# Optimization experiments

Measured on AMD Instinct MI355X. Metric: run time of the kernel, lower is better.

## Reference

```python
import jax, jax.numpy as jnp
import numpy as np
from jax import lax

EPS = 1e-20


def _conv(x, w, pad):
    # x: [B,C,H,W], w: [O,I,kh,kw]
    return lax.conv_general_dilated(
        x, w, window_strides=(1, 1), padding=[(pad, pad), (pad, pad)],
        dimension_numbers=('NCHW', 'OIHW', 'NCHW'))


def _softplus10(p):
    # F.softplus(p, beta=10) = log(1 + exp(10 p)) / 10
    return jax.nn.softplus(10.0 * p) / 10.0


def _nconv(data, conf, w_p, b, pad):
    """Normalized convolution: conv(data*conf)/conv(conf) + bias; cout = conv(conf)/sum(W)."""
    w = _softplus10(w_p)                       # enforce positivity
    denom = _conv(conf, w, pad)                # [B,O,H,W]
    nomin = _conv(data * conf, w, pad)
    out = nomin / (denom + EPS) + b[None, :, None, None]
    s = jnp.sum(w, axis=(1, 2, 3))             # per-out-channel kernel sum
    cout = denom / s[None, :, None, None]
    return out, cout


def _pool_ds2(conf, x):
    """2x2 max-pool on conf (returning conf/4) and gather of x at the argmax positions
    (vectorized equivalent of the torch double for-loop unpool-gather)."""
    B, C, H, W = conf.shape
    cw = conf.reshape(B, C, H // 2, 2, W // 2, 2).transpose(0, 1, 2, 4, 3, 5).reshape(B, C, H // 2, W // 2, 4)
    xw = x.reshape(B, C, H // 2, 2, W // 2, 2).transpose(0, 1, 2, 4, 3, 5).reshape(B, C, H // 2, W // 2, 4)
    idx = jnp.argmax(cw, axis=-1)              # first-max, row-major window order (matches torch)
    c_ds = jnp.take_along_axis(cw, idx[..., None], axis=-1)[..., 0] / 4.0
    x_ds = jnp.take_along_axis(xw, idx[..., None], axis=-1)[..., 0]
    return c_ds, x_ds


def _up2(x):
    return jnp.repeat(jnp.repeat(x, 2, axis=2), 2, axis=3)


def _forward(x0, c0, params):
    (w1, b1, w2, b2, w3, b3, w4, b4, w5, b5, w6, b6, w7, b7) = params
    x1, c1 = _nconv(x0, c0, w1, b1, 2)
    x1, c1 = _nconv(x1, c1, w2, b2, 2)
    x1, c1 = _nconv(x1, c1, w3, b3, 2)

    c1_ds, x1_ds = _pool_ds2(c1, x1)
    x2_ds, c2_ds = _nconv(x1_ds, c1_ds, w2, b2, 2)
    x2_ds, c2_ds = _nconv(x2_ds, c2_ds, w3, b3, 2)

    c2_dss, x2_dss = _pool_ds2(c2_ds, x2_ds)
    x3_ds, c3_ds = _nconv(x2_dss, c2_dss, w2, b2, 2)

    c3_dss, x3_dss = _pool_ds2(c3_ds, x3_ds)
    x4_ds, c4_ds = _nconv(x3_dss, c3_dss, w2, b2, 2)

    x4, c4 = _up2(x4_ds), _up2(c4_ds)
    x34_ds, c34_ds = _nconv(jnp.concatenate((x3_ds, x4), 1), jnp.concatenate((c3_ds, c4), 1), w4, b4, 1)

    x34, c34 = _up2(x34_ds), _up2(c34_ds)
    x23_ds, c23_ds = _nconv(jnp.concatenate((x2_ds, x34), 1), jnp.concatenate((c2_ds, c34), 1), w5, b5, 1)

    x23, c23 = _up2(x23_ds), _up2(c23_ds)
    xout, cout = _nconv(jnp.concatenate((x23, x1), 1), jnp.concatenate((c23, c1), 1), w6, b6, 1)
    xout, cout = _nconv(xout, cout, w7, b7, 0)
    return xout, cout


def setup_inputs() -> dict:
    key = jax.random.key(0)
    ks = jax.random.split(key, 16)
    B, C, H, W = 16, 1, 352, 1216
    nc = 2  # in_ch * num_channels
    x0 = jax.random.uniform(ks[0], (B, C, H, W), jnp.float32)
    c0 = jax.random.uniform(ks[1], (B, C, H, W), jnp.float32)

    def wp(k, shape):
        # weight_p = softplus(kaiming-uniform init); sample a positive-ish param directly
        return jax.random.uniform(k, shape, jnp.float32, 0.02, 0.3)

    inp = {
        'x0': x0, 'c0': c0,
        'w1': wp(ks[2], (nc, C, 5, 5)),       'b1': jnp.full((nc,), 0.01, jnp.float32),
        'w2': wp(ks[3], (nc, nc, 5, 5)),      'b2': jnp.full((nc,), 0.01, jnp.float32),
        'w3': wp(ks[4], (nc, nc, 5, 5)),      'b3': jnp.full((nc,), 0.01, jnp.float32),
        'w4': wp(ks[5], (nc, 2 * nc, 3, 3)),  'b4': jnp.full((nc,), 0.01, jnp.float32),
        'w5': wp(ks[6], (nc, 2 * nc, 3, 3)),  'b5': jnp.full((nc,), 0.01, jnp.float32),
        'w6': wp(ks[7], (nc, 2 * nc, 3, 3)),  'b6': jnp.full((nc,), 0.01, jnp.float32),
        'w7': wp(ks[8], (1, nc, 1, 1)),       'b7': jnp.full((1,), 0.01, jnp.float32),
    }
    return inp


def reference(x0, c0, w1, b1, w2, b2, w3, b3, w4, b4, w5, b5, w6, b6, w7, b7):
    return _forward(x0, c0, (w1, b1, w2, b2, w3, b3, w4, b4, w5, b5, w6, b6, w7, b7))
```

## Files before the change

kernel.cpp:

```cpp
#include <hip/hip_runtime.h>
#include <hip/hip_bf16.h>

#define EPSF 1e-20f
typedef __hip_bfloat16 bf16;
typedef unsigned int u32;

__device__ __forceinline__ float rcpf_(float v) { return __builtin_amdgcn_rcpf(v); }
__device__ __forceinline__ float bits2f(u32 b) { union { u32 i; float f; } u; u.i = b; return u.f; }
__device__ __forceinline__ float lo2f(u32 v) { return bits2f(v << 16); }
__device__ __forceinline__ float hi2f(u32 v) { return bits2f(v & 0xffff0000u); }
__device__ __forceinline__ u32 f2us(float f) {
    bf16 h = __float2bfloat16(f);
    unsigned short s;
    __builtin_memcpy(&s, &h, 2);
    return (u32)s;
}
__device__ __forceinline__ uint2 packpx(float x0, float c0, float x1, float c1) {
    return make_uint2(f2us(x0) | (f2us(c0) << 16), f2us(x1) | (f2us(c1) << 16));
}
__device__ __forceinline__ float4 unpk(uint2 v) {
    float x0 = lo2f(v.x), c0 = hi2f(v.x), x1 = lo2f(v.y), c1 = hi2f(v.y);
    return make_float4(x0 * c0, c0, x1 * c1, c1);
}

#define B_ 16
#define H1 352
#define W1 1216
#define H2 176
#define W2 608
#define H3 88
#define W3 304
#define H4 44
#define W4 152

__global__ void prep_weights(const float* w1, const float* w2, const float* w3,
                             const float* w4, const float* w5, const float* w6,
                             const float* w7, float* wb) {
    const float* ptrs[7] = {w1, w2, w3, w4, w5, w6, w7};
    const int ns[7]   = {50, 100, 100, 72, 72, 72, 2};
    const int offs[7] = {0, 96, 256, 416, 544, 672, 800};
    for (int it = 0; it < 7; ++it)
        for (int i = threadIdx.x; i < ns[it]; i += blockDim.x) {
            float z = 10.f * ptrs[it][i];
            float sp = (z > 20.f) ? z : log1pf(expf(z));
            wb[offs[it] + i] = sp * 0.1f;
        }
    __syncthreads();
    if (threadIdx.x == 0) {
        const int souts[7] = {2, 2, 2, 2, 2, 2, 1};
        const int klen[7]  = {25, 50, 50, 36, 36, 36, 2};
        const int soff[7]  = {64, 224, 384, 512, 640, 768, 804};
        for (int it = 0; it < 7; ++it)
            for (int o = 0; o < souts[it]; ++o) {
                float s = 0.f;
                for (int i = 0; i < klen[it]; ++i) s += wb[offs[it] + o * klen[it] + i];
                wb[soff[it] + o] = s;
            }
        for (int o = 0; o < 2; ++o) {
            wb[808 + o] = 1.f / wb[64 + o];
            wb[810 + o] = 1.f / wb[224 + o];
            wb[812 + o] = 1.f / wb[384 + o];
            wb[814 + o] = 1.f / wb[512 + o];
            wb[816 + o] = 1.f / wb[640 + o];
            wb[818 + o] = 1.f / wb[768 + o];
        }
        wb[820] = 1.f / wb[804];
    }
}

#define TDIM 32

__global__ __launch_bounds__(256) void fused_l1pool(
    const float* __restrict__ x0g, const float* __restrict__ c0g,
    const float* __restrict__ wb,
    const float* __restrict__ b1, const float* __restrict__ b2, const float* __restrict__ b3,
    uint2* __restrict__ Apk, uint2* __restrict__ P1pk) {

    __shared__ float4 A1[40 * 41];
    __shared__ float4 U4[36 * 37];
    float2* U2 = (float2*)U4;

    const int tid = threadIdx.x;
    const int base_h = blockIdx.y * TDIM;
    const int base_w = blockIdx.x * TDIM;
    const int b = blockIdx.z;
    const float* xp = x0g + (long)b * (H1 * W1);
    const float* cp = c0g + (long)b * (H1 * W1);

    for (int i = tid; i < 44 * 44; i += 256) {
        int r = i / 44, c = i % 44;
        int gh = base_h - 6 + r, gw = base_w - 6 + c;
        float xv = 0.f, cv = 0.f;
        if (gh >= 0 && gh < H1 && gw >= 0 && gw < W1) {
            long o = (long)gh * W1 + gw;
            xv = xp[o]; cv = cp[o];
        }
        U2[r * 45 + c] = make_float2(xv * cv, cv);
    }
    __syncthreads();

    {
        const float is0 = wb[808], is1 = wb[809];
        const float bb0 = b1[0], bb1 = b1[1];
        for (int i = tid; i < 400; i += 256) {
            int qr = i / 20, qc = i % 20;
            int r0 = 2 * qr, c0 = 2 * qc;
            float acc[2][2][4];
            #pragma unroll
            for (int a = 0; a < 2; ++a)
                #pragma unroll
                for (int o = 0; o < 2; ++o)
                    #pragma unroll
                    for (int k = 0; k < 4; ++k) acc[a][o][k] = 0.f;
            #pragma unroll
            for (int tr = 0; tr < 6; ++tr) {
                float2 t[6];
                #pragma unroll
                for (int j = 0; j < 6; ++j) t[j] = U2[(r0 + tr) * 45 + c0 + j];
                #pragma unroll
                for (int orr = 0; orr < 2; ++orr) {
                    const int dh = tr - orr;
                    if (dh < 0 || dh > 4) continue;
                    #pragma unroll
                    for (int dw = 0; dw < 5; ++dw) {
                        float wA = wb[dh * 5 + dw];
                        float wB = wb[25 + dh * 5 + dw];
                        #pragma unroll
                        for (int oc = 0; oc < 2; ++oc) {
                            float2 v = t[dw + oc];
                            acc[orr][oc][0] = fmaf(wA, v.x, acc[orr][oc][0]);
                            acc[orr][oc][1] = fmaf(wA, v.y, acc[orr][oc][1]);
                            acc[orr][oc][2] = fmaf(wB, v.x, acc[orr][oc][2]);
                            acc[orr][oc][3] = fmaf(wB, v.y, acc[orr][oc][3]);
                        }
                    }
                }
            }
            #pragma unroll
            for (int orr = 0; orr < 2; ++orr)
                #pragma unroll
                for (int oc = 0; oc < 2; ++oc) {
                    int r = r0 + orr, cc = c0 + oc;
                    int gh = base_h - 4 + r, gw = base_w - 4 + cc;
                    float4 out = make_float4(0.f, 0.f, 0.f, 0.f);
                    if (gh >= 0 && gh < H1 && gw >= 0 && gw < W1) {
                        float n0 = acc[orr][oc][0], d0 = acc[orr][oc][1];
                        float n1 = acc[orr][oc][2], d1 = acc[orr][oc][3];
                        float c0v = d0 * is0, x0v = n0 * rcpf_(d0 + EPSF) + bb0;
                        float c1v = d1 * is1, x1v = n1 * rcpf_(d1 + EPSF) + bb1;
                        out = make_float4(x0v * c0v, c0v, x1v * c1v, c1v);
                    }
                    A1[r * 41 + cc] = out;
                }
        }
    }
    __syncthreads();

    {
        const float is0 = wb[810], is1 = wb[811];
        const float bb0 = b2[0], bb1 = b2[1];
        for (int i = tid; i < 324; i += 256) {
            int qr = i / 18, qc = i % 18;
            int r0 = 2 * qr, c0 = 2 * qc;
            float acc[2][2][4];
            #pragma unroll
            for (int a = 0; a < 2; ++a)
                #pragma unroll
                for (int o = 0; o < 2; ++o)
                    #pragma unroll
                    for (int k = 0; k < 4; ++k) acc[a][o][k] = 0.f;
            #pragma unroll
            for (int tr = 0; tr < 6; ++tr) {
                float4 t[6];
                #pragma unroll
                for (int j = 0; j < 6; ++j) t[j] = A1[(r0 + tr) * 41 + c0 + j];
                #pragma unroll
                for (int orr = 0; orr < 2; ++orr) {
                    const int dh = tr - orr;
                    if (dh < 0 || dh > 4) continue;
                    #pragma unroll
                    for (int dw = 0; dw < 5; ++dw) {
                        const int k = dh * 5 + dw;
                        float wa0 = wb[96 + k],  wc0 = wb[121 + k];
                        float wa1 = wb[146 + k], wc1 = wb[171 + k];
                        #pragma unroll
                        for (int oc = 0; oc < 2; ++oc) {
                            float4 v = t[dw + oc];
                            acc[orr][oc][0] = fmaf(wa0, v.x, fmaf(wc0, v.z, acc[orr][oc][0]));
                            acc[orr][oc][1] = fmaf(wa0, v.y, fmaf(wc0, v.w, acc[orr][oc][1]));
                            acc[orr][oc][2] = fmaf(wa1, v.x, fmaf(wc1, v.z, acc[orr][oc][2]));
                            acc[orr][oc][3] = fmaf(wa1, v.y, fmaf(wc1, v.w, acc[orr][oc][3]));
                        }
                    }
                }
            }
            #pragma unroll
            for (int orr = 0; orr < 2; ++orr)
                #pragma unroll
                for (int oc = 0; oc < 2; ++oc) {
                    int r = r0 + orr, cc = c0 + oc;
                    int gh = base_h - 2 + r, gw = base_w - 2 + cc;
                    float4 out = make_float4(0.f, 0.f, 0.f, 0.f);
                    if (gh >= 0 && gh < H1 && gw >= 0 && gw < W1) {
                        float n0 = acc[orr][oc][0], d0 = acc[orr][oc][1];
                        float n1 = acc[orr][oc][2], d1 = acc[orr][oc][3];
                        float c0v = d0 * is0, x0v = n0 * rcpf_(d0 + EPSF) + bb0;
                        float c1v = d1 * is1, x1v = n1 * rcpf_(d1 + EPSF) + bb1;
                        out = make_float4(x0v * c0v, c0v, x1v * c1v, c1v);
                    }
                    U4[r * 37 + cc] = out;
                }
        }
    }
    __syncthreads();

    {
        const float is0 = wb[812], is1 = wb[813];
        const float bb0 = b3[0], bb1 = b3[1];
        const int pr = tid >> 4, pc = tid & 15;
        const int r0 = 2 * pr, c0 = 2 * pc;
        float acc[2][2][4];
        #pragma unroll
        for (int a = 0; a < 2; ++a)
            #pragma unroll
            for (int o = 0; o < 2; ++o)
                #pragma unroll
                for (int k = 0; k < 4; ++k) acc[a][o][k] = 0.f;
        #pragma unroll
        for (int tr = 0; tr < 6; ++tr) {
            float4 t[6];
            #pragma unroll
            for (int j = 0; j < 6; ++j) t[j] = U4[(r0 + tr) * 37 + c0 + j];
            #pragma unroll
            for (int orr = 0; orr < 2; ++orr) {
                const int dh = tr - orr;
                if (dh < 0 || dh > 4) continue;
                #pragma unroll
                for (int dw = 0; dw < 5; ++dw) {
                    const int k = dh * 5 + dw;
                    float wa0 = wb[256 + k], wc0 = wb[281 + k];
                    float wa1 = wb[306 + k], wc1 = wb[331 + k];
                    #pragma unroll
                    for (int oc = 0; oc < 2; ++oc) {
                        float4 v = t[dw + oc];
                        acc[orr][oc][0] = fmaf(wa0, v.x, fmaf(wc0, v.z, acc[orr][oc][0]));
                        acc[orr][oc][1] = fmaf(wa0, v.y, fmaf(wc0, v.w, acc[orr][oc][1]));
                        acc[orr][oc][2] = fmaf(wa1, v.x, fmaf(wc1, v.z, acc[orr][oc][2]));
                        acc[orr][oc][3] = fmaf(wa1, v.y, fmaf(wc1, v.w, acc[orr][oc][3]));
                    }
                }
            }
        }
        float xv[2][4], cv[2][4];
        #pragma unroll
        for (int orr = 0; orr < 2; ++orr)
            #pragma unroll
            for (int oc = 0; oc < 2; ++oc) {
                int q = orr * 2 + oc;
                float n0 = acc[orr][oc][0], d0 = acc[orr][oc][1];
                float n1 = acc[orr][oc][2], d1 = acc[orr][oc][3];
                xv[0][q] = n0 * rcpf_(d0 + EPSF) + bb0;
                xv[1][q] = n1 * rcpf_(d1 + EPSF) + bb1;
                cv[0][q] = d0 * is0;
                cv[1][q] = d1 * is1;
            }
        int fh = base_h + r0, fw = base_w + c0;
        int ph = (base_h >> 1) + pr, pw = (base_w >> 1) + pc;
        uint2 q00 = packpx(xv[0][0], cv[0][0], xv[1][0], cv[1][0]);
        uint2 q01 = packpx(xv[0][1], cv[0][1], xv[1][1], cv[1][1]);
        uint2 q10 = packpx(xv[0][2], cv[0][2], xv[1][2], cv[1][2]);
        uint2 q11 = packpx(xv[0][3], cv[0][3], xv[1][3], cv[1][3]);
        long o0 = (long)b * (H1 * W1) + (long)fh * W1 + fw;
        *reinterpret_cast<uint4*>(Apk + o0)      = make_uint4(q00.x, q00.y, q01.x, q01.y);
        *reinterpret_cast<uint4*>(Apk + o0 + W1) = make_uint4(q10.x, q10.y, q11.x, q11.y);
        float cm0 = cv[0][0], xs0 = xv[0][0];
        if (cv[0][1] > cm0) { cm0 = cv[0][1]; xs0 = xv[0][1]; }
        if (cv[0][2] > cm0) { cm0 = cv[0][2]; xs0 = xv[0][2]; }
        if (cv[0][3] > cm0) { cm0 = cv[0][3]; xs0 = xv[0][3]; }
        float cm1 = cv[1][0], xs1 = xv[1][0];
        if (cv[1][1] > cm1) { cm1 = cv[1][1]; xs1 = xv[1][1]; }
        if (cv[1][2] > cm1) { cm1 = cv[1][2]; xs1 = xv[1][2]; }
        if (cv[1][3] > cm1) { cm1 = cv[1][3]; xs1 = xv[1][3]; }
        P1pk[(long)b * (H2 * W2) + (long)ph * W2 + pw] =
            packpx(xs0, cm0 * 0.25f, xs1, cm1 * 0.25f);
    }
}

__global__ __launch_bounds__(256) void fused_l2(
    const uint2* __restrict__ P1pk, const float* __restrict__ wb,
    const float* __restrict__ b2, const float* __restrict__ b3,
    uint2* __restrict__ Dpk, uint2* __restrict__ P2pk) {

    __shared__ float4 T0[40 * 41];
    __shared__ float4 T1[36 * 37];

    const int tid = threadIdx.x;
    const int base_h = blockIdx.y * 32;
    const int base_w = blockIdx.x * 32;
    const int b = blockIdx.z;
    const long pl = (long)H2 * W2;
    const uint2* ip = P1pk + (long)b * pl;

    for (int i = tid; i < 40 * 40; i += 256) {
        int r = i / 40, c = i % 40;
        int gh = base_h - 4 + r, gw = base_w - 4 + c;
        float4 v = make_float4(0.f, 0.f, 0.f, 0.f);
        if (gh >= 0 && gh < H2 && gw >= 0 && gw < W2)
            v = unpk(ip[(long)gh * W2 + gw]);
        T0[r * 41 + c] = v;
    }
    __syncthreads();

    {
        const float is0 = wb[810], is1 = wb[811];
        const float bb0 = b2[0], bb1 = b2[1];
        for (int i = tid; i < 324; i += 256) {
            int qr = i / 18, qc = i % 18;
            int r0 = 2 * qr, c0 = 2 * qc;
            float acc[2][2][4];
            #pragma unroll
            for (int a = 0; a < 2; ++a)
                #pragma unroll
                for (int o = 0; o < 2; ++o)
                    #pragma unroll
                    for (int k = 0; k < 4; ++k) acc[a][o][k] = 0.f;
            #pragma unroll
            for (int tr = 0; tr < 6; ++tr) {
                float4 t[6];
                #pragma unroll
                for (int j = 0; j < 6; ++j) t[j] = T0[(r0 + tr) * 41 + c0 + j];
                #pragma unroll
                for (int orr = 0; orr < 2; ++orr) {
                    const int dh = tr - orr;
                    if (dh < 0 || dh > 4) continue;
                    #pragma unroll
                    for (int dw = 0; dw < 5; ++dw) {
                        const int k = dh * 5 + dw;
                        float wa0 = wb[96 + k],  wc0 = wb[121 + k];
                        float wa1 = wb[146 + k], wc1 = wb[171 + k];
                        #pragma unroll
                        for (int oc = 0; oc < 2; ++oc) {
                            float4 v = t[dw + oc];
                            acc[orr][oc][0] = fmaf(wa0, v.x, fmaf(wc0, v.z, acc[orr][oc][0]));
                            acc[orr][oc][1] = fmaf(wa0, v.y, fmaf(wc0, v.w, acc[orr][oc][1]));
                            acc[orr][oc][2] = fmaf(wa1, v.x, fmaf(wc1, v.z, acc[orr][oc][2]));
                            acc[orr][oc][3] = fmaf(wa1, v.y, fmaf(wc1, v.w, acc[orr][oc][3]));
                        }
                    }
                }
            }
            #pragma unroll
            for (int orr = 0; orr < 2; ++orr)
                #pragma unroll
                for (int oc = 0; oc < 2; ++oc) {
                    int r = r0 + orr, cc = c0 + oc;
                    int gh = base_h - 2 + r, gw = base_w - 2 + cc;
                    float4 out = make_float4(0.f, 0.f, 0.f, 0.f);
                    if (gh >= 0 && gh < H2 && gw >= 0 && gw < W2) {
                        float n0 = acc[orr][oc][0], d0 = acc[orr][oc][1];
                        float n1 = acc[orr][oc][2], d1 = acc[orr][oc][3];
                        float c0v = d0 * is0, x0v = n0 * rcpf_(d0 + EPSF) + bb0;
                        float c1v = d1 * is1, x1v = n1 * rcpf_(d1 + EPSF) + bb1;
                        out = make_float4(x0v * c0v, c0v, x1v * c1v, c1v);
                    }
                    T1[r * 37 + cc] = out;
                }
        }
    }
    __syncthreads();

    {
        const float is0 = wb[812], is1 = wb[813];
        const float bb0 = b3[0], bb1 = b3[1];
        const int pr = tid >> 4, pc = tid & 15;
        const int r0 = 2 * pr, c0 = 2 * pc;
        float acc[2][2][4];
        #pragma unroll
        for (int a = 0; a < 2; ++a)
            #pragma unroll
            for (int o = 0; o < 2; ++o)
                #pragma unroll
                for (int k = 0; k < 4; ++k) acc[a][o][k] = 0.f;
        #pragma unroll
        for (int tr = 0; tr < 6; ++tr) {
            float4 t[6];
            #pragma unroll
            for (int j = 0; j < 6; ++j) t[j] = T1[(r0 + tr) * 37 + c0 + j];
            #pragma unroll
            for (int orr = 0; orr < 2; ++orr) {
                const int dh = tr - orr;
                if (dh < 0 || dh > 4) continue;
                #pragma unroll
                for (int dw = 0; dw < 5; ++dw) {
                    const int k = dh * 5 + dw;
                    float wa0 = wb[256 + k], wc0 = wb[281 + k];
                    float wa1 = wb[306 + k], wc1 = wb[331 + k];
                    #pragma unroll
                    for (int oc = 0; oc < 2; ++oc) {
                        float4 v = t[dw + oc];
                        acc[orr][oc][0] = fmaf(wa0, v.x, fmaf(wc0, v.z, acc[orr][oc][0]));
                        acc[orr][oc][1] = fmaf(wa0, v.y, fmaf(wc0, v.w, acc[orr][oc][1]));
                        acc[orr][oc][2] = fmaf(wa1, v.x, fmaf(wc1, v.z, acc[orr][oc][2]));
                        acc[orr][oc][3] = fmaf(wa1, v.y, fmaf(wc1, v.w, acc[orr][oc][3]));
                    }
                }
            }
        }
        int fh = base_h + r0, fw = base_w + c0;
        if (fh < H2) {
            float xv[2][4], cv[2][4];
            #pragma unroll
            for (int orr = 0; orr < 2; ++orr)
                #pragma unroll
                for (int oc = 0; oc < 2; ++oc) {
                    int q = orr * 2 + oc;
                    float n0 = acc[orr][oc][0], d0 = acc[orr][oc][1];
                    float n1 = acc[orr][oc][2], d1 = acc[orr][oc][3];
                    xv[0][q] = n0 * rcpf_(d0 + EPSF) + bb0;
                    xv[1][q] = n1 * rcpf_(d1 + EPSF) + bb1;
                    cv[0][q] = d0 * is0;
                    cv[1][q] = d1 * is1;
                }
            uint2 q00 = packpx(xv[0][0], cv[0][0], xv[1][0], cv[1][0]);
            uint2 q01 = packpx(xv[0][1], cv[0][1], xv[1][1], cv[1][1]);
            uint2 q10 = packpx(xv[0][2], cv[0][2], xv[1][2], cv[1][2]);
            uint2 q11 = packpx(xv[0][3], cv[0][3], xv[1][3], cv[1][3]);
            long o0 = (long)b * pl + (long)fh * W2 + fw;
            *reinterpret_cast<uint4*>(Dpk + o0)      = make_uint4(q00.x, q00.y, q01.x, q01.y);
            *reinterpret_cast<uint4*>(Dpk + o0 + W2) = make_uint4(q10.x, q10.y, q11.x, q11.y);
            float cm0 = cv[0][0], xs0 = xv[0][0];
            if (cv[0][1] > cm0) { cm0 = cv[0][1]; xs0 = xv[0][1]; }
            if (cv[0][2] > cm0) { cm0 = cv[0][2]; xs0 = xv[0][2]; }
            if (cv[0][3] > cm0) { cm0 = cv[0][3]; xs0 = xv[0][3]; }
            float cm1 = cv[1][0], xs1 = xv[1][0];
            if (cv[1][1] > cm1) { cm1 = cv[1][1]; xs1 = xv[1][1]; }
            if (cv[1][2] > cm1) { cm1 = cv[1][2]; xs1 = xv[1][2]; }
            if (cv[1][3] > cm1) { cm1 = cv[1][3]; xs1 = xv[1][3]; }
            int ph = (base_h >> 1) + pr, pw = (base_w >> 1) + pc;
            P2pk[(long)b * (H3 * W3) + (long)ph * W3 + pw] =
                packpx(xs0, cm0 * 0.25f, xs1, cm1 * 0.25f);
        }
    }
}

__global__ __launch_bounds__(256) void fused_l3(
    const uint2* __restrict__ P2pk, const float* __restrict__ wb,
    const float* __restrict__ b2,
    uint2* __restrict__ Gpk, uint2* __restrict__ P3pk) {

    __shared__ float4 T0[36 * 37];

    const int tid = threadIdx.x;
    const int base_h = blockIdx.y * 32;
    const int base_w = blockIdx.x * 32;
    const int b = blockIdx.z;
    const long pl = (long)H3 * W3;
    const uint2* ip = P2pk + (long)b * pl;

    for (int i = tid; i < 36 * 36; i += 256) {
        int r = i / 36, c = i % 36;
        int gh = base_h - 2 + r, gw = base_w - 2 + c;
        float4 v = make_float4(0.f, 0.f, 0.f, 0.f);
        if (gh >= 0 && gh < H3 && gw >= 0 && gw < W3)
            v = unpk(ip[(long)gh * W3 + gw]);
        T0[r * 37 + c] = v;
    }
    __syncthreads();

    {
        const float is0 = wb[810], is1 = wb[811];
        const float bb0 = b2[0], bb1 = b2[1];
        const int pr = tid >> 4, pc = tid & 15;
        const int r0 = 2 * pr, c0 = 2 * pc;
        float acc[2][2][4];
        #pragma unroll
        for (int a = 0; a < 2; ++a)
            #pragma unroll
            for (int o = 0; o < 2; ++o)
                #pragma unroll
                for (int k = 0; k < 4; ++k) acc[a][o][k] = 0.f;
        #pragma unroll
        for (int tr = 0; tr < 6; ++tr) {
            float4 t[6];
            #pragma unroll
            for (int j = 0; j < 6; ++j) t[j] = T0[(r0 + tr) * 37 + c0 + j];
            #pragma unroll
            for (int orr = 0; orr < 2; ++orr) {
                const int dh = tr - orr;
                if (dh < 0 || dh > 4) continue;
                #pragma unroll
                for (int dw = 0; dw < 5; ++dw) {
                    const int k = dh * 5 + dw;
                    float wa0 = wb[96 + k],  wc0 = wb[121 + k];
                    float wa1 = wb[146 + k], wc1 = wb[171 + k];
                    #pragma unroll
                    for (int oc = 0; oc < 2; ++oc) {
                        float4 v = t[dw + oc];
                        acc[orr][oc][0] = fmaf(wa0, v.x, fmaf(wc0, v.z, acc[orr][oc][0]));
                        acc[orr][oc][1] = fmaf(wa0, v.y, fmaf(wc0, v.w, acc[orr][oc][1]));
                        acc[orr][oc][2] = fmaf(wa1, v.x, fmaf(wc1, v.z, acc[orr][oc][2]));
                        acc[orr][oc][3] = fmaf(wa1, v.y, fmaf(wc1, v.w, acc[orr][oc][3]));
                    }
                }
            }
        }
        int fh = base_h + r0, fw = base_w + c0;
        if (fh < H3 && fw < W3) {
            float xv[2][4], cv[2][4];
            #pragma unroll
            for (int orr = 0; orr < 2; ++orr)
                #pragma unroll
                for (int oc = 0; oc < 2; ++oc) {
                    int q = orr * 2 + oc;
                    float n0 = acc[orr][oc][0], d0 = acc[orr][oc][1];
                    float n1 = acc[orr][oc][2], d1 = acc[orr][oc][3];
                    xv[0][q] = n0 * rcpf_(d0 + EPSF) + bb0;
                    xv[1][q] = n1 * rcpf_(d1 + EPSF) + bb1;
                    cv[0][q] = d0 * is0;
                    cv[1][q] = d1 * is1;
                }
            uint2 q00 = packpx(xv[0][0], cv[0][0], xv[1][0], cv[1][0]);
            uint2 q01 = packpx(xv[0][1], cv[0][1], xv[1][1], cv[1][1]);
            uint2 q10 = packpx(xv[0][2], cv[0][2], xv[1][2], cv[1][2]);
            uint2 q11 = packpx(xv[0][3], cv[0][3], xv[1][3], cv[1][3]);
            long o0 = (long)b * pl + (long)fh * W3 + fw;
            *reinterpret_cast<uint4*>(Gpk + o0)      = make_uint4(q00.x, q00.y, q01.x, q01.y);
            *reinterpret_cast<uint4*>(Gpk + o0 + W3) = make_uint4(q10.x, q10.y, q11.x, q11.y);
            float cm0 = cv[0][0], xs0 = xv[0][0];
            if (cv[0][1] > cm0) { cm0 = cv[0][1]; xs0 = xv[0][1]; }
            if (cv[0][2] > cm0) { cm0 = cv[0][2]; xs0 = xv[0][2]; }
            if (cv[0][3] > cm0) { cm0 = cv[0][3]; xs0 = xv[0][3]; }
            float cm1 = cv[1][0], xs1 = xv[1][0];
            if (cv[1][1] > cm1) { cm1 = cv[1][1]; xs1 = xv[1][1]; }
            if (cv[1][2] > cm1) { cm1 = cv[1][2]; xs1 = xv[1][2]; }
            if (cv[1][3] > cm1) { cm1 = cv[1][3]; xs1 = xv[1][3]; }
            int ph = (base_h >> 1) + pr, pw = (base_w >> 1) + pc;
            P3pk[(long)b * (H4 * W4) + (long)ph * W4 + pw] =
                packpx(xs0, cm0 * 0.25f, xs1, cm1 * 0.25f);
        }
    }
}

__global__ void nconv5_pk(const uint2* __restrict__ in, const float* __restrict__ wb,
                          const float* __restrict__ bias, uint2* __restrict__ out,
                          int H, int W) {
    int idx = blockIdx.x * blockDim.x + threadIdx.x;
    int total = B_ * H * W;
    if (idx >= total) return;
    int w = idx % W; int t = idx / W; int h = t % H; int b = t / H;
    const uint2* ip = in + (long)b * H * W;
    float n0 = 0, d0 = 0, n1 = 0, d1 = 0;
    #pragma unroll
    for (int dh = 0; dh < 5; ++dh) {
        int ih = h + dh - 2;
        if (ih < 0 || ih >= H) continue;
        #pragma unroll
        for (int dw = 0; dw < 5; ++dw) {
            int iw = w + dw - 2;
            if (iw < 0 || iw >= W) continue;
// ... 2 lines not shown
            float wa0 = wb[96 + k],  wc0 = wb[121 + k];
            float wa1 = wb[146 + k], wc1 = wb[171 + k];
            n0 = fmaf(wa0, v.x, fmaf(wc0, v.z, n0));
            d0 = fmaf(wa0, v.y, fmaf(wc0, v.w, d0));
            n1 = fmaf(wa1, v.x, fmaf(wc1, v.z, n1));
            d1 = fmaf(wa1, v.y, fmaf(wc1, v.w, d1));
        }
    }
    out[(long)b * H * W + (long)h * W + w] =
        packpx(n0 * rcpf_(d0 + EPSF) + bias[0], d0 * wb[810],
               n1 * rcpf_(d1 + EPSF) + bias[1], d1 * wb[811]);
}

__global__ void nconv_cat_pk(const uint2* __restrict__ nat, const uint2* __restrict__ up,
                             const float* __restrict__ wb, const float* __restrict__ bias,
                             uint2* __restrict__ out, int H, int W) {
    int idx = blockIdx.x * blockDim.x + threadIdx.x;
    int total = B_ * H * W;
    if (idx >= total) return;
    int Hh = H / 2, Wh = W / 2;
    int w = idx % W; int t = idx / W; int h = t % H; int b = t / H;
    const uint2* np = nat + (long)b * H * W;
    const uint2* upp = up + (long)b * Hh * Wh;
    float n0 = 0, d0 = 0, n1 = 0, d1 = 0;
    #pragma unroll
    for (int dh = 0; dh < 3; ++dh) {
        int ih = h + dh - 1;
        if (ih < 0 || ih >= H) continue;
        #pragma unroll
        for (int dw = 0; dw < 3; ++dw) {
            int iw = w + dw - 1;
            if (iw < 0 || iw >= W) continue;
            float4 aN = unpk(np[(long)ih * W + iw]);
            float4 eU = unpk(upp[(long)(ih >> 1) * Wh + (iw >> 1)]);
            const int k = dh * 3 + dw;
            float na0 = wb[416 + k], nb0 = wb[425 + k], ua0 = wb[434 + k], ub0 = wb[443 + k];
            float na1 = wb[452 + k], nb1 = wb[461 + k], ua1 = wb[470 + k], ub1 = wb[479 + k];
            n0 = fmaf(na0, aN.x, fmaf(nb0, aN.z, fmaf(ua0, eU.x, fmaf(ub0, eU.z, n0))));
            d0 = fmaf(na0, aN.y, fmaf(nb0, aN.w, fmaf(ua0, eU.y, fmaf(ub0, eU.w, d0))));
            n1 = fmaf(na1, aN.x, fmaf(nb1, aN.z, fmaf(ua1, eU.x, fmaf(ub1, eU.z, n1))));
            d1 = fmaf(na1, aN.y, fmaf(nb1, aN.w, fmaf(ua1, eU.y, fmaf(ub1, eU.w, d1))));
        }
    }
    out[(long)b * H * W + (long)h * W + w] =
        packpx(n0 * rcpf_(d0 + EPSF) + bias[0], d0 * wb[814],
               n1 * rcpf_(d1 + EPSF) + bias[1], d1 * wb[815]);
}

__global__ __launch_bounds__(256) void nconv_cat_h2t(
    const uint2* __restrict__ Dpk, const uint2* __restrict__ Fpk,
    const float* __restrict__ wb, const float* __restrict__ b5,
    uint2* __restrict__ Epk) {

    __shared__ float4 aT[34 * 35];
    __shared__ float4 eT[18 * 19];

    const int tid = threadIdx.x;
    const int bh = blockIdx.y * 32, bw = blockIdx.x * 32, b = blockIdx.z;
    const int eh0 = (bh - 1) >> 1, ew0 = (bw - 1) >> 1;
    const uint2* dp = Dpk + (long)b * (H2 * W2);
    const uint2* fp = Fpk + (long)b * (H3 * W3);

    for (int i = tid; i < 34 * 34; i += 256) {
        int r = i / 34, c = i % 34;
        int gh = bh - 1 + r, gw = bw - 1 + c;
        float4 v = make_float4(0.f, 0.f, 0.f, 0.f);
        if (gh >= 0 && gh < H2 && gw >= 0 && gw < W2)
            v = unpk(dp[(long)gh * W2 + gw]);
        aT[r * 35 + c] = v;
    }
    for (int i = tid; i < 18 * 18; i += 256) {
        int r = i / 18, c = i % 18;
        int gh = eh0 + r, gw = ew0 + c;
        float4 v = make_float4(0.f, 0.f, 0.f, 0.f);
        if (gh >= 0 && gh < H3 && gw >= 0 && gw < W3)
            v = unpk(fp[(long)gh * W3 + gw]);
        eT[r * 19 + c] = v;
    }
    __syncthreads();

    const int pr = tid >> 4, pc = tid & 15;
    const int r0 = 2 * pr, c0 = 2 * pc;
    float4 a4[4][4], e3[3][3];
    #pragma unroll
    for (int j = 0; j < 4; ++j)
        #pragma unroll
        for (int k = 0; k < 4; ++k) a4[j][k] = aT[(r0 + j) * 35 + c0 + k];
    #pragma unroll
    for (int j = 0; j < 3; ++j)
        #pragma unroll
        for (int k = 0; k < 3; ++k) e3[j][k] = eT[(pr + j) * 19 + pc + k];

    float acc[2][2][4];
    #pragma unroll
    for (int a = 0; a < 2; ++a)
        #pragma unroll
        for (int o = 0; o < 2; ++o)
            #pragma unroll
            for (int k = 0; k < 4; ++k) acc[a][o][k] = 0.f;

    #pragma unroll
    for (int orr = 0; orr < 2; ++orr)
        #pragma unroll
        for (int dh = 0; dh < 3; ++dh)
            #pragma unroll
            for (int oc = 0; oc < 2; ++oc)
                #pragma unroll
                for (int dw = 0; dw < 3; ++dw) {
                    float4 aN = a4[orr + dh][oc + dw];
                    float4 eU = e3[(orr + dh + 1) >> 1][(oc + dw + 1) >> 1];
                    const int k = dh * 3 + dw;
                    float na0 = wb[544 + k], nb0 = wb[553 + k], ua0 = wb[562 + k], ub0 = wb[571 + k];
                    float na1 = wb[580 + k], nb1 = wb[589 + k], ua1 = wb[598 + k], ub1 = wb[607 + k];
                    acc[orr][oc][0] = fmaf(na0, aN.x, fmaf(nb0, aN.z, fmaf(ua0, eU.x, fmaf(ub0, eU.z, acc[orr][oc][0]))));
                    acc[orr][oc][1] = fmaf(na0, aN.y, fmaf(nb0, aN.w, fmaf(ua0, eU.y, fmaf(ub0, eU.w, acc[orr][oc][1]))));
                    acc[orr][oc][2] = fmaf(na1, aN.x, fmaf(nb1, aN.z, fmaf(ua1, eU.x, fmaf(ub1, eU.z, acc[orr][oc][2]))));
                    acc[orr][oc][3] = fmaf(na1, aN.y, fmaf(nb1, aN.w, fmaf(ua1, eU.y, fmaf(ub1, eU.w, acc[orr][oc][3]))));
                }

    int fh = bh + r0, fw = bw + c0;
    if (fh < H2) {
        const float is0 = wb[816], is1 = wb[817];
        const float bb0 = b5[0], bb1 = b5[1];
        float xv[2][4], cv[2][4];
        #pragma unroll
        for (int orr = 0; orr < 2; ++orr)
            #pragma unroll
            for (int oc = 0; oc < 2; ++oc) {
                int q = orr * 2 + oc;
                float n0 = acc[orr][oc][0], d0 = acc[orr][oc][1];
                float n1 = acc[orr][oc][2], d1 = acc[orr][oc][3];
                xv[0][q] = n0 * rcpf_(d0 + EPSF) + bb0;
                xv[1][q] = n1 * rcpf_(d1 + EPSF) + bb1;
                cv[0][q] = d0 * is0;
                cv[1][q] = d1 * is1;
            }
        uint2 q00 = packpx(xv[0][0], cv[0][0], xv[1][0], cv[1][0]);
        uint2 q01 = packpx(xv[0][1], cv[0][1], xv[1][1], cv[1][1]);
        uint2 q10 = packpx(xv[0][2], cv[0][2], xv[1][2], cv[1][2]);
        uint2 q11 = packpx(xv[0][3], cv[0][3], xv[1][3], cv[1][3]);
        long o0 = (long)b * (H2 * W2) + (long)fh * W2 + fw;
        *reinterpret_cast<uint4*>(Epk + o0)      = make_uint4(q00.x, q00.y, q01.x, q01.y);
        *reinterpret_cast<uint4*>(Epk + o0 + W2) = make_uint4(q10.x, q10.y, q11.x, q11.y);
    }
}

__global__ __launch_bounds__(256) void final_tiled(
    const uint2* __restrict__ Apk, const uint2* __restrict__ Epk,
    const float* __restrict__ wb,
    const float* __restrict__ b6g, const float* __restrict__ b7g,
    float* __restrict__ oX, float* __restrict__ oC) {

    __shared__ float4 aT[34 * 35];
    __shared__ float4 eT[18 * 19];

    const int tid = threadIdx.x;
    const int bh = blockIdx.y * 32, bw = blockIdx.x * 32, b = blockIdx.z;
    const int eh0 = (bh - 1) >> 1, ew0 = (bw - 1) >> 1;
    const uint2* ap = Apk + (long)b * (H1 * W1);
    const uint2* ep = Epk + (long)b * (H2 * W2);

    for (int i = tid; i < 34 * 34; i += 256) {
        int r = i / 34, c = i % 34;
        int gh = bh - 1 + r, gw = bw - 1 + c;
        float4 v = make_float4(0.f, 0.f, 0.f, 0.f);
        if (gh >= 0 && gh < H1 && gw >= 0 && gw < W1)
            v = unpk(ap[(long)gh * W1 + gw]);
        aT[r * 35 + c] = v;
    }
    for (int i = tid; i < 18 * 18; i += 256) {
        int r = i / 18, c = i % 18;
        int gh = eh0 + r, gw = ew0 + c;
        float4 v = make_float4(0.f, 0.f, 0.f, 0.f);
        if (gh >= 0 && gh < H2 && gw >= 0 && gw < W2)
            v = unpk(ep[(long)gh * W2 + gw]);
        eT[r * 19 + c] = v;
    }
    __syncthreads();

    const int pr = tid >> 4, pc = tid & 15;
    const int r0 = 2 * pr, c0 = 2 * pc;
    float4 a4[4][4], e3[3][3];
    #pragma unroll
    for (int j = 0; j < 4; ++j)
        #pragma unroll
        for (int k = 0; k < 4; ++k) a4[j][k] = aT[(r0 + j) * 35 + c0 + k];
    #pragma unroll
    for (int j = 0; j < 3; ++j)
        #pragma unroll
        for (int k = 0; k < 3; ++k) e3[j][k] = eT[(pr + j) * 19 + pc + k];

    float acc[2][2][4];
    #pragma unroll
    for (int a = 0; a < 2; ++a)
        #pragma unroll
        for (int o = 0; o < 2; ++o)
            #pragma unroll
            for (int k = 0; k < 4; ++k) acc[a][o][k] = 0.f;

    #pragma unroll
    for (int orr = 0; orr < 2; ++orr)
        #pragma unroll
        for (int dh = 0; dh < 3; ++dh)
            #pragma unroll
            for (int oc = 0; oc < 2; ++oc)
                #pragma unroll
                for (int dw = 0; dw < 3; ++dw) {
                    float4 aN = a4[orr + dh][oc + dw];
                    float4 eU = e3[(orr + dh + 1) >> 1][(oc + dw + 1) >> 1];
                    const int k = dh * 3 + dw;
                    float ua0 = wb[672 + k], ub0 = wb[681 + k], na0 = wb[690 + k], nb0 = wb[699 + k];
                    float ua1 = wb[708 + k], ub1 = wb[717 + k], na1 = wb[726 + k], nb1 = wb[735 + k];
                    acc[orr][oc][0] = fmaf(ua0, eU.x, fmaf(ub0, eU.z, fmaf(na0, aN.x, fmaf(nb0, aN.z, acc[orr][oc][0]))));
                    acc[orr][oc][1] = fmaf(ua0, eU.y, fmaf(ub0, eU.w, fmaf(na0, aN.y, fmaf(nb0, aN.w, acc[orr][oc][1]))));
                    acc[orr][oc][2] = fmaf(ua1, eU.x, fmaf(ub1, eU.z, fmaf(na1, aN.x, fmaf(nb1, aN.z, acc[orr][oc][2]))));
                    acc[orr][oc][3] = fmaf(ua1, eU.y, fmaf(ub1, eU.w, fmaf(na1, aN.y, fmaf(nb1, aN.w, acc[orr][oc][3]))));
                }

    const float is60 = wb[818], is61 = wb[819];
    const float bb60 = b6g[0], bb61 = b6g[1];
    const float w70 = wb[800], w71 = wb[801];
    const float is7 = wb[820], bb7 = b7g[0];
    float ox[2][2], ocv[2][2];
    #pragma unroll
    for (int orr = 0; orr < 2; ++orr)
        #pragma unroll
        for (int oc = 0; oc < 2; ++oc) {
            float n0 = acc[orr][oc][0], d0 = acc[orr][oc][1];
            float n1 = acc[orr][oc][2], d1 = acc[orr][oc][3];
            float x0v = n0 * rcpf_(d0 + EPSF) + bb60;
            float x1v = n1 * rcpf_(d1 + EPSF) + bb61;
            float c0v = d0 * is60, c1v = d1 * is61;
            float den7 = fmaf(w70, c0v, w71 * c1v);
            float nom7 = fmaf(w70, x0v * c0v, w71 * (x1v * c1v));
            ox[orr][oc] = nom7 * rcpf_(den7 + EPSF) + bb7;
            ocv[orr][oc] = den7 * is7;
        }
    long o = (long)b * (H1 * W1) + (long)(bh + r0) * W1 + (bw + c0);
    *reinterpret_cast<float2*>(oX + o)      = make_float2(ox[0][0], ox[0][1]);
    *reinterpret_cast<float2*>(oX + o + W1) = make_float2(ox[1][0], ox[1][1]);
    *reinterpret_cast<float2*>(oC + o)      = make_float2(ocv[0][0], ocv[0][1]);
    *reinterpret_cast<float2*>(oC + o + W1) = make_float2(ocv[1][0], ocv[1][1]);
}

extern "C" void kernel_launch(void* const* d_in, const int* in_sizes, int n_in,
                              void* d_out, int out_size, void* d_ws, size_t ws_size,
                              hipStream_t stream) {
    const float* x0 = (const float*)d_in[0];
    const float* c0 = (const float*)d_in[1];
    const float* w1 = (const float*)d_in[2];
    const float* b1 = (const float*)d_in[3];
    const float* w2 = (const float*)d_in[4];
    const float* b2 = (const float*)d_in[5];
    const float* w3 = (const float*)d_in[6];
    const float* b3 = (const float*)d_in[7];
    const float* w4 = (const float*)d_in[8];
    const float* b4 = (const float*)d_in[9];
    const float* w5 = (const float*)d_in[10];
    const float* b5 = (const float*)d_in[11];
    const float* w6 = (const float*)d_in[12];
    const float* b6 = (const float*)d_in[13];
    const float* w7 = (const float*)d_in[14];
    const float* b7 = (const float*)d_in[15];

    const long N1 = (long)B_ * H1 * W1;
    const long N2 = N1 / 4, N3 = N1 / 16, N4 = N1 / 64;

    float* wb = (float*)d_ws;
    uint2* Apk = (uint2*)((char*)d_ws + 4096);
    uint2* Epk = Apk + N1;

    uint2* R = (uint2*)d_out;
    uint2* P1pk = R;
    uint2* Dpk  = R + N2;
    uint2* P2pk = R + 2 * N2;
    uint2* Gpk  = P2pk + N3;
    uint2* P3pk = Gpk + N3;
    uint2* Ipk  = P3pk + N4;
    uint2* Fpk  = Ipk + N4;

    float* oX = (float*)d_out;
    float* oC = oX + N1;

    prep_weights<<<1, 256, 0, stream>>>(w1, w2, w3, w4, w5, w6, w7, wb);

    dim3 gridF(W1 / TDIM, H1 / TDIM, B_);
    fused_l1pool<<<gridF, 256, 0, stream>>>(x0, c0, wb, b1, b2, b3, Apk, P1pk);

    dim3 gridL2(W2 / 32, (H2 + 31) / 32, B_);
    fused_l2<<<gridL2, 256, 0, stream>>>(P1pk, wb, b2, b3, Dpk, P2pk);

// ... 15 lines not shown
```

Baseline: 448.1 us.

## Split LDS tiles into even/odd column planes to avoid bank conflicts

Shared-memory tiles in all fused stencil kernels are split into separate even-column and odd-column planes. Each thread, whose outputs start at column 2*qc, now reads consecutive addresses across lanes instead of stride-2 float4 addresses, which are meant to avoid LDS bank conflicts. Global tile loads are widened to float2/uint4 where alignment permits, cutting the number of load instructions. Indexing grows more complex, and the wide loads depend on the tile column offsets staying even-aligned.

```diff
diff --git a/kernel.cpp b/kernel.cpp
--- a/kernel.cpp
+++ b/kernel.cpp
@@ -76,26 +76,30 @@
     const float* __restrict__ b1, const float* __restrict__ b2, const float* __restrict__ b3,
     uint2* __restrict__ Apk, uint2* __restrict__ P1pk) {
 
-    __shared__ float4 A1[40 * 41];
-    __shared__ float4 U4[36 * 37];
-    float2* U2 = (float2*)U4;
+    __shared__ float4 A1buf[2 * 40 * 21];
+    __shared__ float4 U4buf[2 * 36 * 19];
+    float4* A1e = A1buf;            float4* A1o = A1buf + 40 * 21;
+    float4* U4e = U4buf;            float4* U4o = U4buf + 36 * 19;
+    float2* U2e = (float2*)U4buf;   float2* U2o = U2e + 44 * 23;
 
     const int tid = threadIdx.x;
     const int base_h = blockIdx.y * TDIM;
     const int base_w = blockIdx.x * TDIM;
     const int b = blockIdx.z;
     const float* xp = x0g + (long)b * (H1 * W1);
-    const float* cp = c0g + (long)b * (H1 * W1);
-
-    for (int i = tid; i < 44 * 44; i += 256) {
-        int r = i / 44, c = i % 44;
-        int gh = base_h - 6 + r, gw = base_w - 6 + c;
-        float xv = 0.f, cv = 0.f;
+    const float* cpg = c0g + (long)b * (H1 * W1);
+
+    for (int i = tid; i < 44 * 22; i += 256) {
+        int r = i / 22, cp2 = i % 22;
+        int gh = base_h - 6 + r, gw = base_w - 6 + 2 * cp2;
+        float2 xv = make_float2(0.f, 0.f), cv = make_float2(0.f, 0.f);
         if (gh >= 0 && gh < H1 && gw >= 0 && gw < W1) {
             long o = (long)gh * W1 + gw;
-            xv = xp[o]; cv = cp[o];
-        }
-        U2[r * 45 + c] = make_float2(xv * cv, cv);
+            xv = *reinterpret_cast<const float2*>(xp + o);
+            cv = *reinterpret_cast<const float2*>(cpg + o);
+        }
+        U2e[r * 23 + cp2] = make_float2(xv.x * cv.x, cv.x);
+        U2o[r * 23 + cp2] = make_float2(xv.y * cv.y, cv.y);
     }
     __syncthreads();
 
@@ -104,7 +108,7 @@
         const float bb0 = b1[0], bb1 = b1[1];
         for (int i = tid; i < 400; i += 256) {
             int qr = i / 20, qc = i % 20;
-            int r0 = 2 * qr, c0 = 2 * qc;
+            int r0 = 2 * qr;
             float acc[2][2][4];
             #pragma unroll
             for (int a = 0; a < 2; ++a)
@@ -114,9 +118,11 @@
                     for (int k = 0; k < 4; ++k) acc[a][o][k] = 0.f;
             #pragma unroll
             for (int tr = 0; tr < 6; ++tr) {
+                const int rr = (r0 + tr) * 23;
                 float2 t[6];
-                #pragma unroll
-                for (int j = 0; j < 6; ++j) t[j] = U2[(r0 + tr) * 45 + c0 + j];
+                t[0] = U2e[rr + qc];     t[1] = U2o[rr + qc];
+                t[2] = U2e[rr + qc + 1]; t[3] = U2o[rr + qc + 1];
+                t[4] = U2e[rr + qc + 2]; t[5] = U2o[rr + qc + 2];
                 #pragma unroll
                 for (int orr = 0; orr < 2; ++orr) {
                     const int dh = tr - orr;
@@ -137,11 +143,12 @@
                 }
             }
             #pragma unroll
-            for (int orr = 0; orr < 2; ++orr)
+            for (int orr = 0; orr < 2; ++orr) {
+                int r = r0 + orr;
+                int gh = base_h - 4 + r;
                 #pragma unroll
                 for (int oc = 0; oc < 2; ++oc) {
-                    int r = r0 + orr, cc = c0 + oc;
-                    int gh = base_h - 4 + r, gw = base_w - 4 + cc;
+                    int gw = base_w - 4 + 2 * qc + oc;
                     float4 out = make_float4(0.f, 0.f, 0.f, 0.f);
                     if (gh >= 0 && gh < H1 && gw >= 0 && gw < W1) {
                         float n0 = acc[orr][oc][0], d0 = acc[orr][oc][1];
@@ -150,8 +157,10 @@
                         float c1v = d1 * is1, x1v = n1 * rcpf_(d1 + EPSF) + bb1;
                         out = make_float4(x0v * c0v, c0v, x1v * c1v, c1v);
                     }
-                    A1[r * 41 + cc] = out;
-                }
+                    if (oc == 0) A1e[r * 21 + qc] = out;
+                    else         A1o[r * 21 + qc] = out;
+                }
+            }
         }
     }
     __syncthreads();
@@ -161,7 +170,7 @@
         const float bb0 = b2[0], bb1 = b2[1];
         for (int i = tid; i < 324; i += 256) {
             int qr = i / 18, qc = i % 18;
-            int r0 = 2 * qr, c0 = 2 * qc;
+            int r0 = 2 * qr;
             float acc[2][2][4];
             #pragma unroll
             for (int a = 0; a < 2; ++a)
@@ -171,9 +180,11 @@
                     for (int k = 0; k < 4; ++k) acc[a][o][k] = 0.f;
             #pragma unroll
             for (int tr = 0; tr < 6; ++tr) {
+                const int rr = (r0 + tr) * 21;
                 float4 t[6];
-                #pragma unroll
-                for (int j = 0; j < 6; ++j) t[j] = A1[(r0 + tr) * 41 + c0 + j];
+                t[0] = A1e[rr + qc];     t[1] = A1o[rr + qc];
+                t[2] = A1e[rr + qc + 1]; t[3] = A1o[rr + qc + 1];
+                t[4] = A1e[rr + qc + 2]; t[5] = A1o[rr + qc + 2];
                 #pragma unroll
                 for (int orr = 0; orr < 2; ++orr) {
                     const int dh = tr - orr;
@@ -195,11 +206,12 @@
                 }
             }
             #pragma unroll
-            for (int orr = 0; orr < 2; ++orr)
+            for (int orr = 0; orr < 2; ++orr) {
+                int r = r0 + orr;
+                int gh = base_h - 2 + r;
                 #pragma unroll
                 for (int oc = 0; oc < 2; ++oc) {
-                    int r = r0 + orr, cc = c0 + oc;
-                    int gh = base_h - 2 + r, gw = base_w - 2 + cc;
+                    int gw = base_w - 2 + 2 * qc + oc;
                     float4 out = make_float4(0.f, 0.f, 0.f, 0.f);
                     if (gh >= 0 && gh < H1 && gw >= 0 && gw < W1) {
                         float n0 = acc[orr][oc][0], d0 = acc[orr][oc][1];
@@ -208,8 +220,10 @@
                         float c1v = d1 * is1, x1v = n1 * rcpf_(d1 + EPSF) + bb1;
                         out = make_float4(x0v * c0v, c0v, x1v * c1v, c1v);
                     }
-                    U4[r * 37 + cc] = out;
-                }
+                    if (oc == 0) U4e[r * 19 + qc] = out;
+                    else         U4o[r * 19 + qc] = out;
+                }
+            }
         }
     }
     __syncthreads();
@@ -218,7 +232,7 @@
         const float is0 = wb[812], is1 = wb[813];
         const float bb0 = b3[0], bb1 = b3[1];
         const int pr = tid >> 4, pc = tid & 15;
-        const int r0 = 2 * pr, c0 = 2 * pc;
+        const int r0 = 2 * pr;
         float acc[2][2][4];
         #pragma unroll
         for (int a = 0; a < 2; ++a)
@@ -228,9 +242,11 @@
                 for (int k = 0; k < 4; ++k) acc[a][o][k] = 0.f;
         #pragma unroll
         for (int tr = 0; tr < 6; ++tr) {
+            const int rr = (r0 + tr) * 19;
             float4 t[6];
-            #pragma unroll
-            for (int j = 0; j < 6; ++j) t[j] = U4[(r0 + tr) * 37 + c0 + j];
+            t[0] = U4e[rr + pc];     t[1] = U4o[rr + pc];
+            t[2] = U4e[rr + pc + 1]; t[3] = U4o[rr + pc + 1];
+            t[4] = U4e[rr + pc + 2]; t[5] = U4o[rr + pc + 2];
             #pragma unroll
             for (int orr = 0; orr < 2; ++orr) {
                 const int dh = tr - orr;
@@ -264,7 +280,7 @@
                 cv[0][q] = d0 * is0;
                 cv[1][q] = d1 * is1;
             }
-        int fh = base_h + r0, fw = base_w + c0;
+        int fh = base_h + r0, fw = base_w + 2 * pc;
         int ph = (base_h >> 1) + pr, pw = (base_w >> 1) + pc;
         uint2 q00 = packpx(xv[0][0], cv[0][0], xv[1][0], cv[1][0]);
         uint2 q01 = packpx(xv[0][1], cv[0][1], xv[1][1], cv[1][1]);
@@ -291,8 +307,10 @@
     const float* __restrict__ b2, const float* __restrict__ b3,
     uint2* __restrict__ Dpk, uint2* __restrict__ P2pk) {
 
-    __shared__ float4 T0[40 * 41];
-    __shared__ float4 T1[36 * 37];
+    __shared__ float4 T0buf[2 * 40 * 21];
+    __shared__ float4 T1buf[2 * 36 * 19];
+    float4* T0e = T0buf; float4* T0o = T0buf + 40 * 21;
+    float4* T1e = T1buf; float4* T1o = T1buf + 36 * 19;
 
     const int tid = threadIdx.x;
     const int base_h = blockIdx.y * 32;
@@ -301,13 +319,14 @@
     const long pl = (long)H2 * W2;
     const uint2* ip = P1pk + (long)b * pl;
 
-    for (int i = tid; i < 40 * 40; i += 256) {
-        int r = i / 40, c = i % 40;
-        int gh = base_h - 4 + r, gw = base_w - 4 + c;
-        float4 v = make_float4(0.f, 0.f, 0.f, 0.f);
+    for (int i = tid; i < 40 * 20; i += 256) {
+        int r = i / 20, cp2 = i % 20;
+        int gh = base_h - 4 + r, gw = base_w - 4 + 2 * cp2;
+        uint4 pp = make_uint4(0, 0, 0, 0);
         if (gh >= 0 && gh < H2 && gw >= 0 && gw < W2)
-            v = unpk(ip[(long)gh * W2 + gw]);
-        T0[r * 41 + c] = v;
+            pp = *reinterpret_cast<const uint4*>(ip + (long)gh * W2 + gw);
+        T0e[r * 21 + cp2] = unpk(make_uint2(pp.x, pp.y));
+        T0o[r * 21 + cp2] = unpk(make_uint2(pp.z, pp.w));
     }
     __syncthreads();
 
@@ -316,7 +335,7 @@
         const float bb0 = b2[0], bb1 = b2[1];
         for (int i = tid; i < 324; i += 256) {
             int qr = i / 18, qc = i % 18;
-            int r0 = 2 * qr, c0 = 2 * qc;
+            int r0 = 2 * qr;
             float acc[2][2][4];
             #pragma unroll
             for (int a = 0; a < 2; ++a)
@@ -326,9 +345,11 @@
                     for (int k = 0; k < 4; ++k) acc[a][o][k] = 0.f;
             #pragma unroll
             for (int tr = 0; tr < 6; ++tr) {
+                const int rr = (r0 + tr) * 21;
                 float4 t[6];
-                #pragma unroll
-                for (int j = 0; j < 6; ++j) t[j] = T0[(r0 + tr) * 41 + c0 + j];
+                t[0] = T0e[rr + qc];     t[1] = T0o[rr + qc];
+                t[2] = T0e[rr + qc + 1]; t[3] = T0o[rr + qc + 1];
+                t[4] = T0e[rr + qc + 2]; t[5] = T0o[rr + qc + 2];
                 #pragma unroll
                 for (int orr = 0; orr < 2; ++orr) {
                     const int dh = tr - orr;
@@ -350,11 +371,12 @@
                 }
             }
             #pragma unroll
-            for (int orr = 0; orr < 2; ++orr)
+            for (int orr = 0; orr < 2; ++orr) {
+                int r = r0 + orr;
+                int gh = base_h - 2 + r;
                 #pragma unroll
                 for (int oc = 0; oc < 2; ++oc) {
-                    int r = r0 + orr, cc = c0 + oc;
-                    int gh = base_h - 2 + r, gw = base_w - 2 + cc;
+                    int gw = base_w - 2 + 2 * qc + oc;
                     float4 out = make_float4(0.f, 0.f, 0.f, 0.f);
                     if (gh >= 0 && gh < H2 && gw >= 0 && gw < W2) {
                         float n0 = acc[orr][oc][0], d0 = acc[orr][oc][1];
@@ -363,8 +385,10 @@
                         float c1v = d1 * is1, x1v = n1 * rcpf_(d1 + EPSF) + bb1;
                         out = make_float4(x0v * c0v, c0v, x1v * c1v, c1v);
                     }
-                    T1[r * 37 + cc] = out;
-                }
+                    if (oc == 0) T1e[r * 19 + qc] = out;
+                    else         T1o[r * 19 + qc] = out;
+                }
+            }
         }
     }
     __syncthreads();
@@ -373,7 +397,7 @@
         const float is0 = wb[812], is1 = wb[813];
         const float bb0 = b3[0], bb1 = b3[1];
         const int pr = tid >> 4, pc = tid & 15;
-        const int r0 = 2 * pr, c0 = 2 * pc;
+        const int r0 = 2 * pr;
         float acc[2][2][4];
         #pragma unroll
         for (int a = 0; a < 2; ++a)
@@ -383,9 +407,11 @@
                 for (int k = 0; k < 4; ++k) acc[a][o][k] = 0.f;
         #pragma unroll
         for (int tr = 0; tr < 6; ++tr) {
+            const int rr = (r0 + tr) * 19;
             float4 t[6];
-            #pragma unroll
-            for (int j = 0; j < 6; ++j) t[j] = T1[(r0 + tr) * 37 + c0 + j];
+            t[0] = T1e[rr + pc];     t[1] = T1o[rr + pc];
+            t[2] = T1e[rr + pc + 1]; t[3] = T1o[rr + pc + 1];
+            t[4] = T1e[rr + pc + 2]; t[5] = T1o[rr + pc + 2];
             #pragma unroll
             for (int orr = 0; orr < 2; ++orr) {
                 const int dh = tr - orr;
@@ -406,7 +432,7 @@
                 }
             }
         }
-        int fh = base_h + r0, fw = base_w + c0;
+        int fh = base_h + r0, fw = base_w + 2 * pc;
         if (fh < H2) {
             float xv[2][4], cv[2][4];
             #pragma unroll
@@ -448,7 +474,8 @@
     const float* __restrict__ b2,
     uint2* __restrict__ Gpk, uint2* __restrict__ P3pk) {
 
-    __shared__ float4 T0[36 * 37];
+    __shared__ float4 T0buf[2 * 36 * 19];
+    float4* T0e = T0buf; float4* T0o = T0buf + 36 * 19;
 
     const int tid = threadIdx.x;
     const int base_h = blockIdx.y * 32;
@@ -457,13 +484,14 @@
     const long pl = (long)H3 * W3;
     const uint2* ip = P2pk + (long)b * pl;
 
-    for (int i = tid; i < 36 * 36; i += 256) {
-        int r = i / 36, c = i % 36;
-        int gh = base_h - 2 + r, gw = base_w - 2 + c;
-        float4 v = make_float4(0.f, 0.f, 0.f, 0.f);
+    for (int i = tid; i < 36 * 18; i += 256) {
+        int r = i / 18, cp2 = i % 18;
+        int gh = base_h - 2 + r, gw = base_w - 2 + 2 * cp2;
+        uint4 pp = make_uint4(0, 0, 0, 0);
         if (gh >= 0 && gh < H3 && gw >= 0 && gw < W3)
-            v = unpk(ip[(long)gh * W3 + gw]);
-        T0[r * 37 + c] = v;
+            pp = *reinterpret_cast<const uint4*>(ip + (long)gh * W3 + gw);
+        T0e[r * 19 + cp2] = unpk(make_uint2(pp.x, pp.y));
+        T0o[r * 19 + cp2] = unpk(make_uint2(pp.z, pp.w));
     }
     __syncthreads();
 
@@ -471,7 +499,7 @@
         const float is0 = wb[810], is1 = wb[811];
         const float bb0 = b2[0], bb1 = b2[1];
         const int pr = tid >> 4, pc = tid & 15;
-        const int r0 = 2 * pr, c0 = 2 * pc;
+        const int r0 = 2 * pr;
         float acc[2][2][4];
         #pragma unroll
         for (int a = 0; a < 2; ++a)
@@ -481,9 +509,11 @@
                 for (int k = 0; k < 4; ++k) acc[a][o][k] = 0.f;
         #pragma unroll
         for (int tr = 0; tr < 6; ++tr) {
+            const int rr = (r0 + tr) * 19;
             float4 t[6];
-            #pragma unroll
-            for (int j = 0; j < 6; ++j) t[j] = T0[(r0 + tr) * 37 + c0 + j];
+            t[0] = T0e[rr + pc];     t[1] = T0o[rr + pc];
+            t[2] = T0e[rr + pc + 1]; t[3] = T0o[rr + pc + 1];
+            t[4] = T0e[rr + pc + 2]; t[5] = T0o[rr + pc + 2];
             #pragma unroll
             for (int orr = 0; orr < 2; ++orr) {
                 const int dh = tr - orr;
@@ -504,7 +534,7 @@
                 }
             }
         }
-        int fh = base_h + r0, fw = base_w + c0;
+        int fh = base_h + r0, fw = base_w + 2 * pc;
         if (fh < H3 && fw < W3) {
             float xv[2][4], cv[2][4];
             #pragma unroll
@@ -613,8 +643,9 @@
     const float* __restrict__ wb, const float* __restrict__ b5,
     uint2* __restrict__ Epk) {
 
-    __shared__ float4 aT[34 * 35];
+    __shared__ float4 aTbuf[2 * 34 * 17];
     __shared__ float4 eT[18 * 19];
+    float4* aTe = aTbuf; float4* aTo = aTbuf + 34 * 17;
 
     const int tid = threadIdx.x;
     const int bh = blockIdx.y * 32, bw = blockIdx.x * 32, b = blockIdx.z;
@@ -622,13 +653,17 @@
     const uint2* dp = Dpk + (long)b * (H2 * W2);
     const uint2* fp = Fpk + (long)b * (H3 * W3);
 
-    for (int i = tid; i < 34 * 34; i += 256) {
-        int r = i / 34, c = i % 34;
-        int gh = bh - 1 + r, gw = bw - 1 + c;
-        float4 v = make_float4(0.f, 0.f, 0.f, 0.f);
-        if (gh >= 0 && gh < H2 && gw >= 0 && gw < W2)
-            v = unpk(dp[(long)gh * W2 + gw]);
-        aT[r * 35 + c] = v;
+    for (int i = tid; i < 34 * 17; i += 256) {
+        int r = i / 17, cp2 = i % 17;
+        int gh = bh - 1 + r;
+        int gw0 = bw - 1 + 2 * cp2, gw1 = gw0 + 1;
+        uint2 p0 = make_uint2(0, 0), p1 = make_uint2(0, 0);
+        if (gh >= 0 && gh < H2) {
+            if (gw0 >= 0 && gw0 < W2) p0 = dp[(long)gh * W2 + gw0];
+            if (gw1 < W2)             p1 = dp[(long)gh * W2 + gw1];
+        }
+        aTe[r * 17 + cp2] = unpk(p0);
+        aTo[r * 17 + cp2] = unpk(p1);
     }
     for (int i = tid; i < 18 * 18; i += 256) {
         int r = i / 18, c = i % 18;
@@ -641,12 +676,14 @@
     __syncthreads();
 
     const int pr = tid >> 4, pc = tid & 15;
-    const int r0 = 2 * pr, c0 = 2 * pc;
+    const int r0 = 2 * pr;
     float4 a4[4][4], e3[3][3];
     #pragma unroll
-    for (int j = 0; j < 4; ++j)
-        #pragma unroll
-        for (int k = 0; k < 4; ++k) a4[j][k] = aT[(r0 + j) * 35 + c0 + k];
+    for (int j = 0; j < 4; ++j) {
+        const int rr = (r0 + j) * 17;
+        a4[j][0] = aTe[rr + pc];     a4[j][1] = aTo[rr + pc];
+        a4[j][2] = aTe[rr + pc + 1]; a4[j][3] = aTo[rr + pc + 1];
+    }
     #pragma unroll
     for (int j = 0; j < 3; ++j)
         #pragma unroll
@@ -679,7 +716,7 @@
                     acc[orr][oc][3] = fmaf(na1, aN.y, fmaf(nb1, aN.w, fmaf(ua1, eU.y, fmaf(ub1, eU.w, acc[orr][oc][3]))));
                 }
 
-    int fh = bh + r0, fw = bw + c0;
+    int fh = bh + r0, fw = bw + 2 * pc;
     if (fh < H2) {
         const float is0 = wb[816], is1 = wb[817];
         const float bb0 = b5[0], bb1 = b5[1];
@@ -712,8 +749,9 @@
     const float* __restrict__ b6g, const float* __restrict__ b7g,
     float* __restrict__ oX, float* __restrict__ oC) {
 
-    __shared__ float4 aT[34 * 35];
+    __shared__ float4 aTbuf[2 * 34 * 17];
     __shared__ float4 eT[18 * 19];
+    float4* aTe = aTbuf; float4* aTo = aTbuf + 34 * 17;
 
     const int tid = threadIdx.x;
     const int bh = blockIdx.y * 32, bw = blockIdx.x * 32, b = blockIdx.z;
@@ -721,13 +759,17 @@
     const uint2* ap = Apk + (long)b * (H1 * W1);
     const uint2* ep = Epk + (long)b * (H2 * W2);
 
-    for (int i = tid; i < 34 * 34; i += 256) {
-        int r = i / 34, c = i % 34;
-        int gh = bh - 1 + r, gw = bw - 1 + c;
-        float4 v = make_float4(0.f, 0.f, 0.f, 0.f);
-        if (gh >= 0 && gh < H1 && gw >= 0 && gw < W1)
-            v = unpk(ap[(long)gh * W1 + gw]);
-        aT[r * 35 + c] = v;
+    for (int i = tid; i < 34 * 17; i += 256) {
+        int r = i / 17, cp2 = i % 17;
+        int gh = bh - 1 + r;
+        int gw0 = bw - 1 + 2 * cp2, gw1 = gw0 + 1;
+        uint2 p0 = make_uint2(0, 0), p1 = make_uint2(0, 0);
+        if (gh >= 0 && gh < H1) {
+            if (gw0 >= 0 && gw0 < W1) p0 = ap[(long)gh * W1 + gw0];
+            if (gw1 < W1)             p1 = ap[(long)gh * W1 + gw1];
+        }
+        aTe[r * 17 + cp2] = unpk(p0);
+        aTo[r * 17 + cp2] = unpk(p1);
     }
     for (int i = tid; i < 18 * 18; i += 256) {
         int r = i / 18, c = i % 18;
@@ -740,12 +782,14 @@
     __syncthreads();
 
     const int pr = tid >> 4, pc = tid & 15;
-    const int r0 = 2 * pr, c0 = 2 * pc;
+    const int r0 = 2 * pr;
     float4 a4[4][4], e3[3][3];
     #pragma unroll
-    for (int j = 0; j < 4; ++j)
-        #pragma unroll
-        for (int k = 0; k < 4; ++k) a4[j][k] = aT[(r0 + j) * 35 + c0 + k];
+    for (int j = 0; j < 4; ++j) {
+        const int rr = (r0 + j) * 17;
+        a4[j][0] = aTe[rr + pc];     a4[j][1] = aTo[rr + pc];
+        a4[j][2] = aTe[rr + pc + 1]; a4[j][3] = aTo[rr + pc + 1];
+    }
     #pragma unroll
     for (int j = 0; j < 3; ++j)
         #pragma unroll
@@ -797,7 +841,7 @@
             ox[orr][oc] = nom7 * rcpf_(den7 + EPSF) + bb7;
             ocv[orr][oc] = den7 * is7;
         }
-    long o = (long)b * (H1 * W1) + (long)(bh + r0) * W1 + (bw + c0);
+    long o = (long)b * (H1 * W1) + (long)(bh + r0) * W1 + (bw + 2 * pc);
     *reinterpret_cast<float2*>(oX + o)      = make_float2(ox[0][0], ox[0][1]);
     *reinterpret_cast<float2*>(oX + o + W1) = make_float2(ox[1][0], ox[1][1]);
     *reinterpret_cast<float2*>(oC + o)      = make_float2(ocv[0][0], ocv[0][1]);
```

After: 422.2 us. -5.8%, faster.
